# Optimization experiments

Hardware: AMD Instinct MI355X
Metric: run time of the kernel (lower is better)

The kernel has to match this reference:

```python
import jax, jax.numpy as jnp
import numpy as np

C = 96          # channels (= output_dim)
NUM_HEADS = 6
DILS = (1, 2, 3)
KS_ATT = 3      # dilate-attention kernel size
KS_COR = 5      # self-correlation kernel size
PAD_COR = 2
LN_EPS = 1e-5


def _unfold(x, k, dil, pad):
    # torch.nn.Unfold(kernel=k, dilation=dil, padding=pad, stride=1)
    # x: [B, C, H, W] -> [B, C, k*k, H, W] (channel-major, kernel row-major)
    B, c, H, W = x.shape
    xp = jnp.pad(x, ((0, 0), (0, 0), (pad, pad), (pad, pad)))
    patches = [xp[:, :, i * dil:i * dil + H, j * dil:j * dil + W]
               for i in range(k) for j in range(k)]
    return jnp.stack(patches, axis=2)


def _layernorm(x, g, b):
    m = jnp.mean(x, axis=-1, keepdims=True)
    v = jnp.mean((x - m) ** 2, axis=-1, keepdims=True)
    return (x - m) * jax.lax.rsqrt(v + LN_EPS) * g + b


def _dilate_attn(q, k, v, dil, head_dim, scale):
    # q,k,v: [B, cb, H, W] with cb = C // num_dilation
    B, cb, H, W = q.shape
    heads = cb // head_dim
    qf = q.reshape(B, heads, head_dim, H * W)                                  # bhdn
    kp = _unfold(k, KS_ATT, dil, dil).reshape(B, heads, head_dim, KS_ATT * KS_ATT, H * W)
    attn = jax.nn.softmax(jnp.einsum('bhdn,bhdkn->bhnk', qf, kp) * scale, axis=-1)
    vp = _unfold(v, KS_ATT, dil, dil).reshape(B, heads, head_dim, KS_ATT * KS_ATT, H * W)
    out = jnp.einsum('bhnk,bhdkn->bnhd', attn, vp)                             # [B,HW,heads,hd]
    return out.reshape(B, H, W, cb)


def _forward(x, g1, b1, Wqkv, bqkv, Wproj, bproj, g2, b2, W1, bm1, W2, bm2):
    B, Cc, H, W = x.shape
    nd = len(DILS)
    head_dim = Cc // NUM_HEADS
    scale = head_dim ** (-0.5)

    xh = jnp.transpose(x, (0, 2, 3, 1))                                        # [B,H,W,C]

    # --- MultiDilatelocalAttention block ---
    y = _layernorm(xh, g1, b1)
    qkv = jnp.einsum('bhwc,oc->bhwo', y, Wqkv) + bqkv                          # 1x1 conv == linear
    qkv = jnp.transpose(qkv, (0, 3, 1, 2)).reshape(B, 3, nd, Cc // nd, H, W)
    outs = []
    for i, d in enumerate(DILS):
        outs.append(_dilate_attn(qkv[:, 0, i], qkv[:, 1, i], qkv[:, 2, i], d, head_dim, scale))
    a = jnp.concatenate(outs, axis=-1)                                         # dilation-major channels
    a = a @ Wproj.T + bproj
    xh = xh + a

    # --- MLP block ---
    z = _layernorm(xh, g2, b2)
    z = jax.nn.gelu(z @ W1.T + bm1, approximate=False) @ W2.T + bm2
    xh = xh + z

    # --- self-correlation ---
    xc = jnp.transpose(xh, (0, 3, 1, 2))                                       # [B,C,H,W]
    xc = jax.nn.relu(xc)
    nrm = jnp.sqrt(jnp.sum(xc * xc, axis=1, keepdims=True))
    xc = xc / jnp.maximum(nrm, 1e-12)                                          # F.normalize dim=1
    pat = _unfold(xc, KS_COR, 1, PAD_COR)                                      # [B,C,25,H,W]
    out = pat.reshape(B, Cc, KS_COR, KS_COR, H, W) * xc[:, :, None, None]
    return jnp.transpose(out, (0, 1, 4, 5, 2, 3))                              # [B,C,H,W,5,5]


def setup_inputs() -> dict:
    key = jax.random.key(0)
    ks = jax.random.split(key, 8)
    B, H, W = 8, 64, 64
    s = 0.02
    return {
        'x': jax.random.normal(ks[0], (B, C, H, W), jnp.float32),
        'g1': jnp.ones((C,), jnp.float32),
        'b1': jnp.zeros((C,), jnp.float32),
        'Wqkv': jax.random.normal(ks[1], (3 * C, C), jnp.float32) * s,
        'bqkv': jnp.zeros((3 * C,), jnp.float32),
        'Wproj': jax.random.normal(ks[2], (C, C), jnp.float32) * s,
        'bproj': jnp.zeros((C,), jnp.float32),
        'g2': jnp.ones((C,), jnp.float32),
        'b2': jnp.zeros((C,), jnp.float32),
        'W1': jax.random.normal(ks[3], (4 * C, C), jnp.float32) * s,
        'bm1': jnp.zeros((4 * C,), jnp.float32),
        'W2': jax.random.normal(ks[4], (C, 4 * C), jnp.float32) * s,
        'bm2': jnp.zeros((C,), jnp.float32),
    }


def reference(x, g1, b1, Wqkv, bqkv, Wproj, bproj, g2, b2, W1, bm1, W2, bm2):
    return _forward(x, g1, b1, Wqkv, bqkv, Wproj, bproj, g2, b2, W1, bm1, W2, bm2)
```

## Files before the change

kernel.cpp:

```cpp
#include <hip/hip_runtime.h>
#include <math.h>

#define NN 4096
#define BN 32768

using short8 = __attribute__((ext_vector_type(8))) short;
using f32x4  = __attribute__((ext_vector_type(4))) float;
typedef unsigned short ushort_t;

__device__ inline ushort_t f2bf(float f) {
    unsigned u = __builtin_bit_cast(unsigned, f);
    u += 0x7FFFu + ((u >> 16) & 1u);
    return (ushort_t)(u >> 16);
}
__device__ inline float bf2f(ushort_t h) {
    unsigned u = ((unsigned)h) << 16;
    return __builtin_bit_cast(float, u);
}

__global__ __launch_bounds__(256) void k1_ln_qkv(
    const float* __restrict__ x, const float* __restrict__ g1, const float* __restrict__ b1,
    const float* __restrict__ Wqkv, const float* __restrict__ bqkv,
    float* __restrict__ xh, ushort_t* __restrict__ qkvt)
{
    __shared__ __align__(16) float    Cs[96 * 69];
    __shared__ __align__(16) ushort_t As[64 * 104];
    __shared__ __align__(16) ushort_t Bs[96 * 104];
    const int tid = threadIdx.x;
    const long bn0 = (long)blockIdx.x * 64;
    const int b = (int)(bn0 >> 12);
    const int hw0 = (int)(bn0 & 4095);
    const float* xb = x + ((long)b * 96 * NN + hw0);

    for (int i = 0; i < 24; ++i) {
        int idx = i * 256 + tid;
        int c = idx >> 6, p = idx & 63;
        Cs[c * 69 + p] = xb[(long)c * NN + p];
    }
    __syncthreads();
    for (int i = 0; i < 6; ++i) {
        int idx = i * 256 + tid;
        int p = idx / 24, c4 = idx % 24;
        float4 v = make_float4(Cs[(4*c4+0)*69 + p], Cs[(4*c4+1)*69 + p],
                               Cs[(4*c4+2)*69 + p], Cs[(4*c4+3)*69 + p]);
        *(float4*)&xh[(bn0 + p) * 96 + 4*c4] = v;
    }
    __syncthreads();
    {
        int p = tid >> 2, part = tid & 3, c0 = part * 24;
        float s = 0.f, ss = 0.f;
        for (int c = c0; c < c0 + 24; ++c) { float v = Cs[c*69 + p]; s += v; ss += v*v; }
        s  += __shfl_xor(s, 1);  s  += __shfl_xor(s, 2);
        ss += __shfl_xor(ss, 1); ss += __shfl_xor(ss, 2);
        float m = s * (1.f/96.f);
        float rstd = rsqrtf(ss * (1.f/96.f) - m*m + 1e-5f);
        for (int c = c0; c < c0 + 24; ++c)
            Cs[c*69 + p] = (Cs[c*69 + p] - m) * rstd * g1[c] + b1[c];
    }
    __syncthreads();
    for (int i = 0; i < 12; ++i) {
        int idx = i * 256 + tid;
        int p = idx / 48, cp = idx % 48;
        unsigned lo = f2bf(Cs[(2*cp  )*69 + p]);
        unsigned hi = f2bf(Cs[(2*cp+1)*69 + p]);
        *(unsigned*)&As[p * 104 + 2*cp] = lo | (hi << 16);
    }

    const int lane = tid & 63, wv = tid >> 6;
    const int ln = lane & 15, qd = lane >> 4;
    for (int ch = 0; ch < 3; ++ch) {
        __syncthreads();
        for (int i = 0; i < 18; ++i) {
            int idx = i * 256 + tid;
            int o = idx / 48, cp = idx % 48;
            const float* wp = Wqkv + (long)(ch*96 + o)*96 + 2*cp;
            unsigned lo = f2bf(wp[0]), hi = f2bf(wp[1]);
            *(unsigned*)&Bs[o * 104 + 2*cp] = lo | (hi << 16);
        }
        __syncthreads();
        f32x4 acc[6];
        #pragma unroll
        for (int t = 0; t < 6; ++t) acc[t] = (f32x4){0.f, 0.f, 0.f, 0.f};
        #pragma unroll
        for (int kc = 0; kc < 3; ++kc) {
            short8 a = *(const short8*)&As[(wv*16 + ln)*104 + kc*32 + qd*8];
            #pragma unroll
            for (int t = 0; t < 6; ++t) {
                short8 bf = *(const short8*)&Bs[(t*16 + ln)*104 + kc*32 + qd*8];
                acc[t] = __builtin_amdgcn_mfma_f32_16x16x32_bf16(a, bf, acc[t], 0, 0, 0);
            }
        }
        #pragma unroll
        for (int t = 0; t < 6; ++t)
            #pragma unroll
            for (int r = 0; r < 4; ++r)
                Cs[(t*16 + ln)*69 + (wv*16 + qd*4 + r)] = acc[t][r];
        __syncthreads();
        for (int i = 0; i < 12; ++i) {
            int idx = i * 256 + tid;
            int c = idx / 32, ph = idx % 32;
            float bias = bqkv[ch*96 + c];
            unsigned lo = f2bf(Cs[c*69 + 2*ph    ] + bias);
            unsigned hi = f2bf(Cs[c*69 + 2*ph + 1] + bias);
            *(unsigned*)&qkvt[(((long)(b*288 + ch*96 + c)) << 12) + hw0 + 2*ph] = lo | (hi << 16);
        }
    }
}

__global__ __launch_bounds__(256) void k2_attn(
    const ushort_t* __restrict__ qkvt, ushort_t* __restrict__ abt)
{
    int t = blockIdx.x * 256 + threadIdx.x;
    int n = t & 4095;
    int r = t >> 12;
    int head = r & 1;
    int di = (r >> 1) % 3;
    int b = r / 6;
    int h = n >> 6, w = n & 63;
    int dil = di + 1;
    const int cg = di*32 + head*16;
    const long planeQ = ((long)(b*288 +       cg)) << 12;
    const long planeK = ((long)(b*288 +  96 + cg)) << 12;
    const long planeV = ((long)(b*288 + 192 + cg)) << 12;

    float q[16];
    #pragma unroll
    for (int d = 0; d < 16; ++d) q[d] = bf2f(qkvt[planeQ + ((long)d << 12) + n]);

    float logits[9];
    #pragma unroll
    for (int ki = 0; ki < 3; ++ki)
        #pragma unroll
        for (int kj = 0; kj < 3; ++kj) {
            int hh = h + (ki-1)*dil, ww = w + (kj-1)*dil;
            float l = 0.f;
            if ((unsigned)hh < 64u && (unsigned)ww < 64u) {
                int nn = (hh << 6) + ww;
                #pragma unroll
                for (int d = 0; d < 16; ++d)
                    l += q[d] * bf2f(qkvt[planeK + ((long)d << 12) + nn]);
            }
            logits[ki*3 + kj] = l * 0.25f;
        }
    float m = logits[0];
    #pragma unroll
    for (int k = 1; k < 9; ++k) m = fmaxf(m, logits[k]);
    float e[9], s = 0.f;
    #pragma unroll
    for (int k = 0; k < 9; ++k) { e[k] = expf(logits[k] - m); s += e[k]; }
    float inv = 1.f / s;

    float o[16];
    #pragma unroll
    for (int d = 0; d < 16; ++d) o[d] = 0.f;
    #pragma unroll
    for (int ki = 0; ki < 3; ++ki)
        #pragma unroll
        for (int kj = 0; kj < 3; ++kj) {
            int hh = h + (ki-1)*dil, ww = w + (kj-1)*dil;
            if ((unsigned)hh < 64u && (unsigned)ww < 64u) {
                int nn = (hh << 6) + ww;
                float wgt = e[ki*3 + kj] * inv;
                #pragma unroll
                for (int d = 0; d < 16; ++d)
                    o[d] += wgt * bf2f(qkvt[planeV + ((long)d << 12) + nn]);
            }
        }
    const long ob = ((long)(b*96 + cg)) << 12;
    #pragma unroll
    for (int d = 0; d < 16; ++d)
        abt[ob + ((long)d << 12) + n] = f2bf(o[d]);
}

__global__ __launch_bounds__(256) void k3_proj_ln(
    const ushort_t* __restrict__ abt, const float* __restrict__ Wproj, const float* __restrict__ bproj,
    const float* __restrict__ g2, const float* __restrict__ b2,
    float* __restrict__ xh, ushort_t* __restrict__ zt)
{
    __shared__ __align__(16) float    Cs[96 * 69];
    __shared__ __align__(16) ushort_t As[64 * 104];
    __shared__ __align__(16) ushort_t Bs[96 * 104];
    __shared__ float lnm[64], lnr[64];
    const int tid = threadIdx.x;
    const long bn0 = (long)blockIdx.x * 64;
    const int b = (int)(bn0 >> 12);
    const int hw0 = (int)(bn0 & 4095);

    for (int i = 0; i < 12; ++i) {
        int idx = i * 256 + tid;
        int c = idx / 32, ph = idx % 32;
        unsigned v = *(const unsigned*)&abt[(((long)(b*96 + c)) << 12) + hw0 + 2*ph];
        As[(2*ph  )*104 + c] = (ushort_t)(v & 0xFFFF);
        As[(2*ph+1)*104 + c] = (ushort_t)(v >> 16);
    }
    for (int i = 0; i < 18; ++i) {
        int idx = i * 256 + tid;
        int o = idx / 48, cp = idx % 48;
        const float* wp = Wproj + (long)o*96 + 2*cp;
        unsigned lo = f2bf(wp[0]), hi = f2bf(wp[1]);
        *(unsigned*)&Bs[o * 104 + 2*cp] = lo | (hi << 16);
    }
    __syncthreads();
    const int lane = tid & 63, wv = tid >> 6;
    const int ln = lane & 15, qd = lane >> 4;
    f32x4 acc[6];
    #pragma unroll
    for (int t = 0; t < 6; ++t) acc[t] = (f32x4){0.f, 0.f, 0.f, 0.f};
    #pragma unroll
    for (int kc = 0; kc < 3; ++kc) {
        short8 a = *(const short8*)&As[(wv*16 + ln)*104 + kc*32 + qd*8];
        #pragma unroll
        for (int t = 0; t < 6; ++t) {
            short8 bf = *(const short8*)&Bs[(t*16 + ln)*104 + kc*32 + qd*8];
            acc[t] = __builtin_amdgcn_mfma_f32_16x16x32_bf16(a, bf, acc[t], 0, 0, 0);
        }
    }
    #pragma unroll
    for (int t = 0; t < 6; ++t)
        #pragma unroll
        for (int r = 0; r < 4; ++r)
            Cs[(t*16 + ln)*69 + (wv*16 + qd*4 + r)] = acc[t][r];
    __syncthreads();
    for (int i = 0; i < 24; ++i) {
        int idx = i * 256 + tid;
        int p = idx / 96, c = idx % 96;
        long g = (bn0 + p) * 96 + c;
        float v = Cs[c*69 + p] + bproj[c] + xh[g];
        xh[g] = v;
        Cs[c*69 + p] = v;
    }
    __syncthreads();
    {
        int p = tid >> 2, part = tid & 3, c0 = part * 24;
        float s = 0.f, ss = 0.f;
        for (int c = c0; c < c0 + 24; ++c) { float v = Cs[c*69 + p]; s += v; ss += v*v; }
        s  += __shfl_xor(s, 1);  s  += __shfl_xor(s, 2);
        ss += __shfl_xor(ss, 1); ss += __shfl_xor(ss, 2);
        float m = s * (1.f/96.f);
        float rstd = rsqrtf(ss * (1.f/96.f) - m*m + 1e-5f);
        if (part == 0) { lnm[p] = m; lnr[p] = rstd; }
    }
    __syncthreads();
    for (int i = 0; i < 12; ++i) {
        int idx = i * 256 + tid;
        int p = idx / 48, cp = idx % 48;
        float m = lnm[p], rs = lnr[p];
        int c0 = 2*cp;
        float v0 = (Cs[(c0  )*69 + p] - m) * rs * g2[c0  ] + b2[c0  ];
        float v1 = (Cs[(c0+1)*69 + p] - m) * rs * g2[c0+1] + b2[c0+1];
        unsigned lo = f2bf(v0), hi = f2bf(v1);
        *(unsigned*)&zt[(bn0 + p) * 96 + c0] = lo | (hi << 16);
    }
}

__global__ __launch_bounds__(256) void k4_mlp1(
    const ushort_t* __restrict__ zt, const float* __restrict__ W1, const float* __restrict__ bm1,
    ushort_t* __restrict__ hbt)
{
    __shared__ __align__(16) float    Cs[96 * 69];
    __shared__ __align__(16) ushort_t As[64 * 104];
    __shared__ __align__(16) ushort_t Bs[96 * 104];
    const int tid = threadIdx.x;
    const long bn0 = (long)blockIdx.x * 64;
    const int ch = blockIdx.y;

    for (int i = 0; i < 12; ++i) {
        int idx = i * 256 + tid;
        int p = idx / 48, cp = idx % 48;
        *(unsigned*)&As[p * 104 + 2*cp] = *(const unsigned*)&zt[(bn0 + p) * 96 + 2*cp];
    }
    for (int i = 0; i < 18; ++i) {
        int idx = i * 256 + tid;
        int o = idx / 48, cp = idx % 48;
        const float* wp = W1 + (long)(ch*96 + o)*96 + 2*cp;
        unsigned lo = f2bf(wp[0]), hi = f2bf(wp[1]);
        *(unsigned*)&Bs[o * 104 + 2*cp] = lo | (hi << 16);
    }
    __syncthreads();
    const int lane = tid & 63, wv = tid >> 6;
    const int ln = lane & 15, qd = lane >> 4;
    f32x4 acc[6];
    #pragma unroll
    for (int t = 0; t < 6; ++t) acc[t] = (f32x4){0.f, 0.f, 0.f, 0.f};
    #pragma unroll
    for (int kc = 0; kc < 3; ++kc) {
        short8 a = *(const short8*)&As[(wv*16 + ln)*104 + kc*32 + qd*8];
        #pragma unroll
        for (int t = 0; t < 6; ++t) {
            short8 bf = *(const short8*)&Bs[(t*16 + ln)*104 + kc*32 + qd*8];
            acc[t] = __builtin_amdgcn_mfma_f32_16x16x32_bf16(a, bf, acc[t], 0, 0, 0);
        }
    }
    #pragma unroll
    for (int t = 0; t < 6; ++t)
        #pragma unroll
        for (int r = 0; r < 4; ++r)
            Cs[(t*16 + ln)*69 + (wv*16 + qd*4 + r)] = acc[t][r];
    __syncthreads();
    for (int i = 0; i < 12; ++i) {
        int idx = i * 256 + tid;
        int p = idx / 48, cp = idx % 48;
        int c0 = 2*cp;
        float v0 = Cs[(c0  )*69 + p] + bm1[ch*96 + c0  ];
        float v1 = Cs[(c0+1)*69 + p] + bm1[ch*96 + c0+1];
        v0 = 0.5f * v0 * (1.f + erff(v0 * 0.70710678118654752f));
        v1 = 0.5f * v1 * (1.f + erff(v1 * 0.70710678118654752f));
        unsigned lo = f2bf(v0), hi = f2bf(v1);
        *(unsigned*)&hbt[(bn0 + p) * 384 + ch*96 + c0] = lo | (hi << 16);
    }
}

__global__ __launch_bounds__(256) void k5_mlp2_norm(
    const ushort_t* __restrict__ hbt, const float* __restrict__ W2, const float* __restrict__ bm2,
    const float* __restrict__ xh, float* __restrict__ xcn)
{
    __shared__ __align__(16) float    Cs[96 * 69];
    __shared__ __align__(16) ushort_t As[64 * 104];
    __shared__ __align__(16) ushort_t Bs[96 * 104];
    __shared__ float lnr[64];
    const int tid = threadIdx.x;
    const long bn0 = (long)blockIdx.x * 64;
    const int lane = tid & 63, wv = tid >> 6;
    const int ln = lane & 15, qd = lane >> 4;
    f32x4 acc[6];
    #pragma unroll
    for (int t = 0; t < 6; ++t) acc[t] = (f32x4){0.f, 0.f, 0.f, 0.f};

    for (int kb = 0; kb < 4; ++kb) {
        __syncthreads();
        for (int i = 0; i < 12; ++i) {
            int idx = i * 256 + tid;
            int p = idx / 48, cp = idx % 48;
            *(unsigned*)&As[p * 104 + 2*cp] =
                *(const unsigned*)&hbt[(bn0 + p) * 384 + kb*96 + 2*cp];
        }
        for (int i = 0; i < 18; ++i) {
            int idx = i * 256 + tid;
            int o = idx / 48, cp = idx % 48;
            const float* wp = W2 + (long)o*384 + kb*96 + 2*cp;
            unsigned lo = f2bf(wp[0]), hi = f2bf(wp[1]);
            *(unsigned*)&Bs[o * 104 + 2*cp] = lo | (hi << 16);
        }
        __syncthreads();
        #pragma unroll
        for (int kc = 0; kc < 3; ++kc) {
            short8 a = *(const short8*)&As[(wv*16 + ln)*104 + kc*32 + qd*8];
            #pragma unroll
            for (int t = 0; t < 6; ++t) {
                short8 bf = *(const short8*)&Bs[(t*16 + ln)*104 + kc*32 + qd*8];
                acc[t] = __builtin_amdgcn_mfma_f32_16x16x32_bf16(a, bf, acc[t], 0, 0, 0);
            }
        }
    }
    #pragma unroll
    for (int t = 0; t < 6; ++t)
        #pragma unroll
        for (int r = 0; r < 4; ++r)
            Cs[(t*16 + ln)*69 + (wv*16 + qd*4 + r)] = acc[t][r];
    __syncthreads();
    for (int i = 0; i < 24; ++i) {
        int idx = i * 256 + tid;
        int p = idx / 96, c = idx % 96;
        float v = Cs[c*69 + p] + bm2[c] + xh[(bn0 + p) * 96 + c];
        Cs[c*69 + p] = fmaxf(v, 0.f);
    }
    __syncthreads();
    {
        int p = tid >> 2, part = tid & 3, c0 = part * 24;
        float ss = 0.f;
        for (int c = c0; c < c0 + 24; ++c) { float v = Cs[c*69 + p]; ss += v*v; }
        ss += __shfl_xor(ss, 1); ss += __shfl_xor(ss, 2);
        if (part == 0) lnr[p] = 1.f / fmaxf(sqrtf(ss), 1e-12f);
    }
    __syncthreads();
    for (int i = 0; i < 12; ++i) {
        int idx = i * 256 + tid;
        int p = idx / 48, cp = idx % 48;
        float inv = lnr[p];
        float2 v = make_float2(Cs[(2*cp)*69 + p] * inv, Cs[(2*cp+1)*69 + p] * inv);
        *(float2*)&xcn[(bn0 + p) * 96 + 2*cp] = v;
    }
}

__global__ __launch_bounds__(256) void k6_selfcorr(
    const float* __restrict__ xcn, float* __restrict__ out)
{
    __shared__ float xt[5 * 20 * 97];
    const int tid = threadIdx.x;
    const int wc = blockIdx.x;
    const int h  = blockIdx.y;
    const int b  = blockIdx.z;
    const int w0 = wc * 16;

    for (int i = 0; i < 38; ++i) {
        int idx = i * 256 + tid;
        if (idx < 9600) {
            int r = idx / (20 * 96);
            int rem = idx - r * (20 * 96);
            int wi = rem / 96, c = rem - wi * 96;
            int hh = h + r - 2, ww = w0 + wi - 2;
            float v = 0.f;
            if ((unsigned)hh < 64u && (unsigned)ww < 64u)
                v = xcn[(((long)b << 12) + (hh << 6) + ww) * 96 + c];
            xt[(r * 20 + wi) * 97 + c] = v;
        }
    }
    __syncthreads();
    const long obase = ((long)b * 96 * 4096 + (long)h * 64) * 25;
    for (int i = 0; i < 150; ++i) {
        int o = i * 256 + tid;
        int c = o / 400;
        int r2 = o - c * 400;
        int lw = r2 / 25, k = r2 - lw * 25;
        int ki = k / 5, kj = k - ki * 5;
        float center = xt[(2 * 20 + lw + 2) * 97 + c];
        float neigh  = xt[(ki * 20 + lw + kj) * 97 + c];
        out[obase + (long)c * (4096 * 25) + (w0 + lw) * 25 + k] = center * neigh;
    }
}

extern "C" void kernel_launch(void* const* d_in, const int* in_sizes, int n_in,
                              void* d_out, int out_size, void* d_ws, size_t ws_size,
                              hipStream_t stream)
{
    const float* x     = (const float*)d_in[0];
    const float* g1    = (const float*)d_in[1];
    const float* b1    = (const float*)d_in[2];
    const float* Wqkv  = (const float*)d_in[3];
    const float* bqkv  = (const float*)d_in[4];
    const float* Wproj = (const float*)d_in[5];
    const float* bproj = (const float*)d_in[6];
    const float* g2    = (const float*)d_in[7];
    const float* b2    = (const float*)d_in[8];
    const float* W1    = (const float*)d_in[9];
    const float* bm1   = (const float*)d_in[10];
    const float* W2    = (const float*)d_in[11];
    const float* bm2   = (const float*)d_in[12];
    float* out = (float*)d_out;

    char* w = (char*)d_ws;
    float*    xh   = (float*)w;    w += (size_t)BN * 96  * 4;
    float*    xcn  = (float*)w;    w += (size_t)BN * 96  * 4;
    ushort_t* qkvt = (ushort_t*)w; w += (size_t)BN * 288 * 2;
    ushort_t* abt  = (ushort_t*)w; w += (size_t)BN * 96  * 2;
    ushort_t* zt   = (ushort_t*)w; w += (size_t)BN * 96  * 2;
    ushort_t* hbt  = (ushort_t*)w;

    k1_ln_qkv   <<<BN / 64, 256, 0, stream>>>(x, g1, b1, Wqkv, bqkv, xh, qkvt);
    k2_attn     <<<(BN * 6) / 256, 256, 0, stream>>>(qkvt, abt);
    k3_proj_ln  <<<BN / 64, 256, 0, stream>>>(abt, Wproj, bproj, g2, b2, xh, zt);
    k4_mlp1     <<<dim3(BN / 64, 4), 256, 0, stream>>>(zt, W1, bm1, hbt);
    k5_mlp2_norm<<<BN / 64, 256, 0, stream>>>(hbt, W2, bm2, xh, xcn);
    k6_selfcorr <<<dim3(4, 64, 8), 256, 0, stream>>>(xcn, out);
}
```

Before: 492.8 us.

## Fuse proj, MLP and norm kernels, pre-convert weights, pack bf16 pairs

Adds a prologue kernel that converts all weights to bf16 once per call. Fuses the projection+LN, MLP1 and MLP2+norm kernels into one, which keeps the hidden activations in shared memory and reloads the residual from x instead of a separate xh buffer. It also packs channel pairs into 32-bit words for the qkv and attention buffers to halve the number of loads in attention. The self-correlation output is now written with float4 stores. The fused kernel serialises the four MLP chunks within each block and uses more shared memory and registers, which may reduce occupancy.

```diff
diff --git a/kernel.cpp b/kernel.cpp
--- a/kernel.cpp
+++ b/kernel.cpp
@@ -13,15 +13,34 @@
     u += 0x7FFFu + ((u >> 16) & 1u);
     return (ushort_t)(u >> 16);
 }
+__device__ inline float bflo(unsigned u) {
+    return __builtin_bit_cast(float, u << 16);
+}
+__device__ inline float bfhi(unsigned u) {
+    return __builtin_bit_cast(float, u & 0xFFFF0000u);
+}
 __device__ inline float bf2f(ushort_t h) {
-    unsigned u = ((unsigned)h) << 16;
-    return __builtin_bit_cast(float, u);
+    return __builtin_bit_cast(float, ((unsigned)h) << 16);
+}
+
+__global__ __launch_bounds__(256) void k0_cvt(
+    const float* __restrict__ Wqkv, const float* __restrict__ Wproj,
+    const float* __restrict__ W1, const float* __restrict__ W2,
+    ushort_t* __restrict__ wb)
+{
+    int i = blockIdx.x * 256 + threadIdx.x;
+    float v;
+    if (i < 27648)      v = Wqkv[i];
+    else if (i < 36864) v = Wproj[i - 27648];
+    else if (i < 73728) v = W1[i - 36864];
+    else                v = W2[i - 73728];
+    wb[i] = f2bf(v);
 }
 
 __global__ __launch_bounds__(256) void k1_ln_qkv(
     const float* __restrict__ x, const float* __restrict__ g1, const float* __restrict__ b1,
-    const float* __restrict__ Wqkv, const float* __restrict__ bqkv,
-    float* __restrict__ xh, ushort_t* __restrict__ qkvt)
+    const ushort_t* __restrict__ wqkv_b, const float* __restrict__ bqkv,
+    unsigned* __restrict__ qkvt32)
 {
     __shared__ __align__(16) float    Cs[96 * 69];
     __shared__ __align__(16) ushort_t As[64 * 104];
@@ -29,21 +48,13 @@
     const int tid = threadIdx.x;
     const long bn0 = (long)blockIdx.x * 64;
     const int b = (int)(bn0 >> 12);
-    const int hw0 = (int)(bn0 & 4095);
-    const float* xb = x + ((long)b * 96 * NN + hw0);
+    const int n0 = (int)(bn0 & 4095);
+    const unsigned* wqkv32 = (const unsigned*)wqkv_b;
 
     for (int i = 0; i < 24; ++i) {
         int idx = i * 256 + tid;
         int c = idx >> 6, p = idx & 63;
-        Cs[c * 69 + p] = xb[(long)c * NN + p];
-    }
-    __syncthreads();
-    for (int i = 0; i < 6; ++i) {
-        int idx = i * 256 + tid;
-        int p = idx / 24, c4 = idx % 24;
-        float4 v = make_float4(Cs[(4*c4+0)*69 + p], Cs[(4*c4+1)*69 + p],
-                               Cs[(4*c4+2)*69 + p], Cs[(4*c4+3)*69 + p]);
-        *(float4*)&xh[(bn0 + p) * 96 + 4*c4] = v;
+        Cs[c * 69 + p] = x[((long)(b * 96 + c) << 12) + n0 + p];
     }
     __syncthreads();
     {
@@ -73,9 +84,7 @@
         for (int i = 0; i < 18; ++i) {
             int idx = i * 256 + tid;
             int o = idx / 48, cp = idx % 48;
-            const float* wp = Wqkv + (long)(ch*96 + o)*96 + 2*cp;
-            unsigned lo = f2bf(wp[0]), hi = f2bf(wp[1]);
-            *(unsigned*)&Bs[o * 104 + 2*cp] = lo | (hi << 16);
+            *(unsigned*)&Bs[o * 104 + 2*cp] = wqkv32[(ch*96 + o)*48 + cp];
         }
         __syncthreads();
         f32x4 acc[6];
@@ -98,17 +107,18 @@
         __syncthreads();
         for (int i = 0; i < 12; ++i) {
             int idx = i * 256 + tid;
-            int c = idx / 32, ph = idx % 32;
-            float bias = bqkv[ch*96 + c];
-            unsigned lo = f2bf(Cs[c*69 + 2*ph    ] + bias);
-            unsigned hi = f2bf(Cs[c*69 + 2*ph + 1] + bias);
-            *(unsigned*)&qkvt[(((long)(b*288 + ch*96 + c)) << 12) + hw0 + 2*ph] = lo | (hi << 16);
+            int cp = idx / 64, p = idx % 64;
+            int c = 2*cp;
+            float b0v = bqkv[ch*96 + c], b1v = bqkv[ch*96 + c + 1];
+            unsigned lo = f2bf(Cs[c*69 + p] + b0v);
+            unsigned hi = f2bf(Cs[(c+1)*69 + p] + b1v);
+            qkvt32[((long)(b*144 + ch*48 + cp) << 12) + n0 + p] = lo | (hi << 16);
         }
     }
 }
 
 __global__ __launch_bounds__(256) void k2_attn(
-    const ushort_t* __restrict__ qkvt, ushort_t* __restrict__ abt)
+    const unsigned* __restrict__ qkvt32, unsigned* __restrict__ abt32)
 {
     int t = blockIdx.x * 256 + threadIdx.x;
     int n = t & 4095;
@@ -118,14 +128,17 @@
     int b = r / 6;
     int h = n >> 6, w = n & 63;
     int dil = di + 1;
-    const int cg = di*32 + head*16;
-    const long planeQ = ((long)(b*288 +       cg)) << 12;
-    const long planeK = ((long)(b*288 +  96 + cg)) << 12;
-    const long planeV = ((long)(b*288 + 192 + cg)) << 12;
+    const int cp0 = di*16 + head*8;
+    const unsigned* Q = qkvt32 + ((long)(b*144 +      cp0) << 12);
+    const unsigned* K = qkvt32 + ((long)(b*144 + 48 + cp0) << 12);
+    const unsigned* V = qkvt32 + ((long)(b*144 + 96 + cp0) << 12);
 
     float q[16];
     #pragma unroll
-    for (int d = 0; d < 16; ++d) q[d] = bf2f(qkvt[planeQ + ((long)d << 12) + n]);
+    for (int j = 0; j < 8; ++j) {
+        unsigned u = Q[((long)j << 12) + n];
+        q[2*j] = bflo(u); q[2*j+1] = bfhi(u);
+    }
 
     float logits[9];
     #pragma unroll
@@ -137,8 +150,10 @@
             if ((unsigned)hh < 64u && (unsigned)ww < 64u) {
                 int nn = (hh << 6) + ww;
                 #pragma unroll
-                for (int d = 0; d < 16; ++d)
-                    l += q[d] * bf2f(qkvt[planeK + ((long)d << 12) + nn]);
+                for (int j = 0; j < 8; ++j) {
+                    unsigned u = K[((long)j << 12) + nn];
+                    l += q[2*j] * bflo(u) + q[2*j+1] * bfhi(u);
+                }
             }
             logits[ki*3 + kj] = l * 0.25f;
         }
@@ -162,71 +177,81 @@
                 int nn = (hh << 6) + ww;
                 float wgt = e[ki*3 + kj] * inv;
                 #pragma unroll
-                for (int d = 0; d < 16; ++d)
-                    o[d] += wgt * bf2f(qkvt[planeV + ((long)d << 12) + nn]);
-            }
-        }
-    const long ob = ((long)(b*96 + cg)) << 12;
-    #pragma unroll
-    for (int d = 0; d < 16; ++d)
-        abt[ob + ((long)d << 12) + n] = f2bf(o[d]);
-}
-
-__global__ __launch_bounds__(256) void k3_proj_ln(
-    const ushort_t* __restrict__ abt, const float* __restrict__ Wproj, const float* __restrict__ bproj,
+                for (int j = 0; j < 8; ++j) {
+                    unsigned u = V[((long)j << 12) + nn];
+                    o[2*j]   += wgt * bflo(u);
+                    o[2*j+1] += wgt * bfhi(u);
+                }
+            }
+        }
+    #pragma unroll
+    for (int j = 0; j < 8; ++j) {
+        unsigned lo = f2bf(o[2*j]), hi = f2bf(o[2*j+1]);
+        abt32[((long)(b*48 + cp0 + j) << 12) + n] = lo | (hi << 16);
+    }
+}
+
+__global__ __launch_bounds__(256) void k345(
+    const unsigned* __restrict__ abt32, const float* __restrict__ x,
+    const ushort_t* __restrict__ wproj_b, const float* __restrict__ bproj,
     const float* __restrict__ g2, const float* __restrict__ b2,
-    float* __restrict__ xh, ushort_t* __restrict__ zt)
+    const ushort_t* __restrict__ w1_b, const float* __restrict__ bm1,
+    const ushort_t* __restrict__ w2_b, const float* __restrict__ bm2,
+    float* __restrict__ xcn)
 {
     __shared__ __align__(16) float    Cs[96 * 69];
     __shared__ __align__(16) ushort_t As[64 * 104];
+    __shared__ __align__(16) ushort_t Ah[64 * 104];
     __shared__ __align__(16) ushort_t Bs[96 * 104];
     __shared__ float lnm[64], lnr[64];
     const int tid = threadIdx.x;
     const long bn0 = (long)blockIdx.x * 64;
     const int b = (int)(bn0 >> 12);
-    const int hw0 = (int)(bn0 & 4095);
-
-    for (int i = 0; i < 12; ++i) {
-        int idx = i * 256 + tid;
-        int c = idx / 32, ph = idx % 32;
-        unsigned v = *(const unsigned*)&abt[(((long)(b*96 + c)) << 12) + hw0 + 2*ph];
-        As[(2*ph  )*104 + c] = (ushort_t)(v & 0xFFFF);
-        As[(2*ph+1)*104 + c] = (ushort_t)(v >> 16);
-    }
-    for (int i = 0; i < 18; ++i) {
-        int idx = i * 256 + tid;
-        int o = idx / 48, cp = idx % 48;
-        const float* wp = Wproj + (long)o*96 + 2*cp;
-        unsigned lo = f2bf(wp[0]), hi = f2bf(wp[1]);
-        *(unsigned*)&Bs[o * 104 + 2*cp] = lo | (hi << 16);
-    }
-    __syncthreads();
+    const int n0 = (int)(bn0 & 4095);
+    const unsigned* wproj32 = (const unsigned*)wproj_b;
+    const unsigned* w1_32   = (const unsigned*)w1_b;
+    const unsigned* w2_32   = (const unsigned*)w2_b;
     const int lane = tid & 63, wv = tid >> 6;
     const int ln = lane & 15, qd = lane >> 4;
-    f32x4 acc[6];
-    #pragma unroll
-    for (int t = 0; t < 6; ++t) acc[t] = (f32x4){0.f, 0.f, 0.f, 0.f};
-    #pragma unroll
-    for (int kc = 0; kc < 3; ++kc) {
-        short8 a = *(const short8*)&As[(wv*16 + ln)*104 + kc*32 + qd*8];
-        #pragma unroll
-        for (int t = 0; t < 6; ++t) {
-            short8 bf = *(const short8*)&Bs[(t*16 + ln)*104 + kc*32 + qd*8];
-            acc[t] = __builtin_amdgcn_mfma_f32_16x16x32_bf16(a, bf, acc[t], 0, 0, 0);
-        }
-    }
-    #pragma unroll
-    for (int t = 0; t < 6; ++t)
-        #pragma unroll
-        for (int r = 0; r < 4; ++r)
-            Cs[(t*16 + ln)*69 + (wv*16 + qd*4 + r)] = acc[t][r];
-    __syncthreads();
+
+    for (int i = 0; i < 12; ++i) {
+        int idx = i * 256 + tid;
+        int cp = idx / 64, p = idx % 64;
+        *(unsigned*)&As[p * 104 + 2*cp] = abt32[((long)(b*48 + cp) << 12) + n0 + p];
+    }
+    for (int i = 0; i < 18; ++i) {
+        int idx = i * 256 + tid;
+        int o = idx / 48, cp = idx % 48;
+        *(unsigned*)&Bs[o * 104 + 2*cp] = wproj32[o*48 + cp];
+    }
+    __syncthreads();
+    {
+        f32x4 acc[6];
+        #pragma unroll
+        for (int t = 0; t < 6; ++t) acc[t] = (f32x4){0.f, 0.f, 0.f, 0.f};
+        #pragma unroll
+        for (int kc = 0; kc < 3; ++kc) {
+            short8 a = *(const short8*)&As[(wv*16 + ln)*104 + kc*32 + qd*8];
+            #pragma unroll
+            for (int t = 0; t < 6; ++t) {
+                short8 bf = *(const short8*)&Bs[(t*16 + ln)*104 + kc*32 + qd*8];
+                acc[t] = __builtin_amdgcn_mfma_f32_16x16x32_bf16(a, bf, acc[t], 0, 0, 0);
+            }
+        }
+        #pragma unroll
+        for (int t = 0; t < 6; ++t)
+            #pragma unroll
+            for (int r = 0; r < 4; ++r)
+                Cs[(t*16 + ln)*69 + (wv*16 + qd*4 + r)] = acc[t][r];
+    }
+    __syncthreads();
+    float resid[24];
+    #pragma unroll
     for (int i = 0; i < 24; ++i) {
         int idx = i * 256 + tid;
-        int p = idx / 96, c = idx % 96;
-        long g = (bn0 + p) * 96 + c;
-        float v = Cs[c*69 + p] + bproj[c] + xh[g];
-        xh[g] = v;
+        int c = idx >> 6, p = idx & 63;
+        float v = Cs[c*69 + p] + bproj[c] + x[((long)(b*96 + c) << 12) + n0 + p];
+        resid[i] = v;
         Cs[c*69 + p] = v;
     }
     __syncthreads();
@@ -245,123 +270,74 @@
         int idx = i * 256 + tid;
         int p = idx / 48, cp = idx % 48;
         float m = lnm[p], rs = lnr[p];
-        int c0 = 2*cp;
-        float v0 = (Cs[(c0  )*69 + p] - m) * rs * g2[c0  ] + b2[c0  ];
-        float v1 = (Cs[(c0+1)*69 + p] - m) * rs * g2[c0+1] + b2[c0+1];
-        unsigned lo = f2bf(v0), hi = f2bf(v1);
-        *(unsigned*)&zt[(bn0 + p) * 96 + c0] = lo | (hi << 16);
-    }
-}
-
-__global__ __launch_bounds__(256) void k4_mlp1(
-    const ushort_t* __restrict__ zt, const float* __restrict__ W1, const float* __restrict__ bm1,
-    ushort_t* __restrict__ hbt)
-{
-    __shared__ __align__(16) float    Cs[96 * 69];
-    __shared__ __align__(16) ushort_t As[64 * 104];
-    __shared__ __align__(16) ushort_t Bs[96 * 104];
-    const int tid = threadIdx.x;
-    const long bn0 = (long)blockIdx.x * 64;
-    const int ch = blockIdx.y;
-
-    for (int i = 0; i < 12; ++i) {
-        int idx = i * 256 + tid;
-        int p = idx / 48, cp = idx % 48;
-        *(unsigned*)&As[p * 104 + 2*cp] = *(const unsigned*)&zt[(bn0 + p) * 96 + 2*cp];
-    }
-    for (int i = 0; i < 18; ++i) {
-        int idx = i * 256 + tid;
-        int o = idx / 48, cp = idx % 48;
-        const float* wp = W1 + (long)(ch*96 + o)*96 + 2*cp;
-        unsigned lo = f2bf(wp[0]), hi = f2bf(wp[1]);
-        *(unsigned*)&Bs[o * 104 + 2*cp] = lo | (hi << 16);
-    }
-    __syncthreads();
-    const int lane = tid & 63, wv = tid >> 6;
-    const int ln = lane & 15, qd = lane >> 4;
-    f32x4 acc[6];
-    #pragma unroll
-    for (int t = 0; t < 6; ++t) acc[t] = (f32x4){0.f, 0.f, 0.f, 0.f};
-    #pragma unroll
-    for (int kc = 0; kc < 3; ++kc) {
-        short8 a = *(const short8*)&As[(wv*16 + ln)*104 + kc*32 + qd*8];
-        #pragma unroll
-        for (int t = 0; t < 6; ++t) {
-            short8 bf = *(const short8*)&Bs[(t*16 + ln)*104 + kc*32 + qd*8];
-            acc[t] = __builtin_amdgcn_mfma_f32_16x16x32_bf16(a, bf, acc[t], 0, 0, 0);
-        }
-    }
-    #pragma unroll
-    for (int t = 0; t < 6; ++t)
-        #pragma unroll
-        for (int r = 0; r < 4; ++r)
-            Cs[(t*16 + ln)*69 + (wv*16 + qd*4 + r)] = acc[t][r];
-    __syncthreads();
-    for (int i = 0; i < 12; ++i) {
-        int idx = i * 256 + tid;
-        int p = idx / 48, cp = idx % 48;
-        int c0 = 2*cp;
-        float v0 = Cs[(c0  )*69 + p] + bm1[ch*96 + c0  ];
-        float v1 = Cs[(c0+1)*69 + p] + bm1[ch*96 + c0+1];
-        v0 = 0.5f * v0 * (1.f + erff(v0 * 0.70710678118654752f));
-        v1 = 0.5f * v1 * (1.f + erff(v1 * 0.70710678118654752f));
-        unsigned lo = f2bf(v0), hi = f2bf(v1);
-        *(unsigned*)&hbt[(bn0 + p) * 384 + ch*96 + c0] = lo | (hi << 16);
-    }
-}
-
-__global__ __launch_bounds__(256) void k5_mlp2_norm(
-    const ushort_t* __restrict__ hbt, const float* __restrict__ W2, const float* __restrict__ bm2,
-    const float* __restrict__ xh, float* __restrict__ xcn)
-{
-    __shared__ __align__(16) float    Cs[96 * 69];
-    __shared__ __align__(16) ushort_t As[64 * 104];
-    __shared__ __align__(16) ushort_t Bs[96 * 104];
-    __shared__ float lnr[64];
-    const int tid = threadIdx.x;
-    const long bn0 = (long)blockIdx.x * 64;
-    const int lane = tid & 63, wv = tid >> 6;
-    const int ln = lane & 15, qd = lane >> 4;
-    f32x4 acc[6];
-    #pragma unroll
-    for (int t = 0; t < 6; ++t) acc[t] = (f32x4){0.f, 0.f, 0.f, 0.f};
-
+        int c = 2*cp;
+        unsigned lo = f2bf((Cs[(c  )*69 + p] - m) * rs * g2[c  ] + b2[c  ]);
+        unsigned hi = f2bf((Cs[(c+1)*69 + p] - m) * rs * g2[c+1] + b2[c+1]);
+        *(unsigned*)&As[p * 104 + 2*cp] = lo | (hi << 16);
+    }
+
+    f32x4 acc2[6];
+    #pragma unroll
+    for (int t = 0; t < 6; ++t) acc2[t] = (f32x4){0.f, 0.f, 0.f, 0.f};
     for (int kb = 0; kb < 4; ++kb) {
         __syncthreads();
-        for (int i = 0; i < 12; ++i) {
-            int idx = i * 256 + tid;
-            int p = idx / 48, cp = idx % 48;
-            *(unsigned*)&As[p * 104 + 2*cp] =
-                *(const unsigned*)&hbt[(bn0 + p) * 384 + kb*96 + 2*cp];
-        }
         for (int i = 0; i < 18; ++i) {
             int idx = i * 256 + tid;
             int o = idx / 48, cp = idx % 48;
-            const float* wp = W2 + (long)o*384 + kb*96 + 2*cp;
-            unsigned lo = f2bf(wp[0]), hi = f2bf(wp[1]);
-            *(unsigned*)&Bs[o * 104 + 2*cp] = lo | (hi << 16);
-        }
-        __syncthreads();
+            *(unsigned*)&Bs[o * 104 + 2*cp] = w1_32[(kb*96 + o)*48 + cp];
+        }
+        __syncthreads();
+        f32x4 acch[6];
+        #pragma unroll
+        for (int t = 0; t < 6; ++t) acch[t] = (f32x4){0.f, 0.f, 0.f, 0.f};
         #pragma unroll
         for (int kc = 0; kc < 3; ++kc) {
             short8 a = *(const short8*)&As[(wv*16 + ln)*104 + kc*32 + qd*8];
             #pragma unroll
             for (int t = 0; t < 6; ++t) {
                 short8 bf = *(const short8*)&Bs[(t*16 + ln)*104 + kc*32 + qd*8];
-                acc[t] = __builtin_amdgcn_mfma_f32_16x16x32_bf16(a, bf, acc[t], 0, 0, 0);
-            }
-        }
-    }
+                acch[t] = __builtin_amdgcn_mfma_f32_16x16x32_bf16(a, bf, acch[t], 0, 0, 0);
+            }
+        }
+        #pragma unroll
+        for (int t = 0; t < 6; ++t) {
+            float bias = bm1[kb*96 + t*16 + ln];
+            #pragma unroll
+            for (int r = 0; r < 4; ++r) {
+                float v = acch[t][r] + bias;
+                v = 0.5f * v * (1.f + erff(v * 0.70710678118654752f));
+                Ah[(wv*16 + qd*4 + r)*104 + t*16 + ln] = f2bf(v);
+            }
+        }
+        __syncthreads();
+        for (int i = 0; i < 18; ++i) {
+            int idx = i * 256 + tid;
+            int o = idx / 48, cp = idx % 48;
+            *(unsigned*)&Bs[o * 104 + 2*cp] = w2_32[o*192 + kb*48 + cp];
+        }
+        __syncthreads();
+        #pragma unroll
+        for (int kc = 0; kc < 3; ++kc) {
+            short8 a = *(const short8*)&Ah[(wv*16 + ln)*104 + kc*32 + qd*8];
+            #pragma unroll
+            for (int t = 0; t < 6; ++t) {
+                short8 bf = *(const short8*)&Bs[(t*16 + ln)*104 + kc*32 + qd*8];
+                acc2[t] = __builtin_amdgcn_mfma_f32_16x16x32_bf16(a, bf, acc2[t], 0, 0, 0);
+            }
+        }
+    }
+    __syncthreads();
     #pragma unroll
     for (int t = 0; t < 6; ++t)
         #pragma unroll
         for (int r = 0; r < 4; ++r)
-            Cs[(t*16 + ln)*69 + (wv*16 + qd*4 + r)] = acc[t][r];
-    __syncthreads();
+            Cs[(t*16 + ln)*69 + (wv*16 + qd*4 + r)] = acc2[t][r];
+    __syncthreads();
+    #pragma unroll
     for (int i = 0; i < 24; ++i) {
         int idx = i * 256 + tid;
-        int p = idx / 96, c = idx % 96;
-        float v = Cs[c*69 + p] + bm2[c] + xh[(bn0 + p) * 96 + c];
+        int c = idx >> 6, p = idx & 63;
+        float v = Cs[c*69 + p] + bm2[c] + resid[i];
         Cs[c*69 + p] = fmaxf(v, 0.f);
     }
     __syncthreads();
@@ -406,16 +382,25 @@
         }
     }
     __syncthreads();
-    const long obase = ((long)b * 96 * 4096 + (long)h * 64) * 25;
-    for (int i = 0; i < 150; ++i) {
-        int o = i * 256 + tid;
-        int c = o / 400;
-        int r2 = o - c * 400;
-        int lw = r2 / 25, k = r2 - lw * 25;
-        int ki = k / 5, kj = k - ki * 5;
-        float center = xt[(2 * 20 + lw + 2) * 97 + c];
-        float neigh  = xt[(ki * 20 + lw + kj) * 97 + c];
-        out[obase + (long)c * (4096 * 25) + (w0 + lw) * 25 + k] = center * neigh;
+    float4* out4 = (float4*)out;
+    const long ob4 = (long)b * 2457600 + (long)h * 400 + wc * 100;
+    for (int i = 0; i < 38; ++i) {
+        int idx = i * 256 + tid;
+        if (idx < 9600) {
+            int c = idx / 100;
+            int r4 = idx - c * 100;
+            float4 v;
+            #pragma unroll
+            for (int j = 0; j < 4; ++j) {
+                int r = r4 * 4 + j;
+                int lw = r / 25, k = r - lw * 25;
+                int ki = k / 5, kj = k - ki * 5;
+                float center = xt[(42 + lw) * 97 + c];
+                float neigh  = xt[(ki * 20 + lw + kj) * 97 + c];
+                (&v.x)[j] = center * neigh;
+            }
+            out4[ob4 + (long)c * 25600 + r4] = v;
+        }
     }
 }
 
@@ -439,17 +424,19 @@
     float* out = (float*)d_out;
 
     char* w = (char*)d_ws;
-    float*    xh   = (float*)w;    w += (size_t)BN * 96  * 4;
-    float*    xcn  = (float*)w;    w += (size_t)BN * 96  * 4;
-    ushort_t* qkvt = (ushort_t*)w; w += (size_t)BN * 288 * 2;
-    ushort_t* abt  = (ushort_t*)w; w += (size_t)BN * 96  * 2;
-    ushort_t* zt   = (ushort_t*)w; w += (size_t)BN * 96  * 2;
-    ushort_t* hbt  = (ushort_t*)w;
-
-    k1_ln_qkv   <<<BN / 64, 256, 0, stream>>>(x, g1, b1, Wqkv, bqkv, xh, qkvt);
-    k2_attn     <<<(BN * 6) / 256, 256, 0, stream>>>(qkvt, abt);
-    k3_proj_ln  <<<BN / 64, 256, 0, stream>>>(abt, Wproj, bproj, g2, b2, xh, zt);
-    k4_mlp1     <<<dim3(BN / 64, 4), 256, 0, stream>>>(zt, W1, bm1, hbt);
-    k5_mlp2_norm<<<BN / 64, 256, 0, stream>>>(hbt, W2, bm2, xh, xcn);
-    k6_selfcorr <<<dim3(4, 64, 8), 256, 0, stream>>>(xcn, out);
-}
+    unsigned* qkvt32 = (unsigned*)w;  w += (size_t)BN * 288 * 2;
+    unsigned* abt32  = (unsigned*)w;  w += (size_t)BN * 96 * 2;
+    float*    xcn    = (float*)w;     w += (size_t)BN * 96 * 4;
+    ushort_t* wb     = (ushort_t*)w;  w += (size_t)110592 * 2;
+    ushort_t* wqkv_b = wb;
+    ushort_t* wproj_b= wb + 27648;
+    ushort_t* w1_b   = wb + 36864;
+    ushort_t* w2_b   = wb + 73728;
+
+    k0_cvt     <<<432, 256, 0, stream>>>(Wqkv, Wproj, W1, W2, wb);
+    k1_ln_qkv  <<<BN / 64, 256, 0, stream>>>(x, g1, b1, wqkv_b, bqkv, qkvt32);
+    k2_attn    <<<(BN * 6) / 256, 256, 0, stream>>>(qkvt32, abt32);
+    k345       <<<BN / 64, 256, 0, stream>>>(abt32, x, wproj_b, bproj, g2, b2,
+                                             w1_b, bm1, w2_b, bm2, xcn);
+    k6_selfcorr<<<dim3(4, 64, 8), 256, 0, stream>>>(xcn, out);
+}
```

After: 479.7 us. 2.7% less time.
